# Kernel optimization log

Hardware: AMD Instinct MI355X
Metric: run time of the kernel (lower is better)

The kernel has to match this reference:

```python
import jax, jax.numpy as jnp
import numpy as np

B, T, I, H, L, O = 256, 256, 512, 1024, 2, 5


def setup_inputs() -> dict:
    key = jax.random.key(0)
    ks = jax.random.split(key, 8)
    x = jax.random.normal(ks[0], (B, T, I), dtype=jnp.float32)
    hidden = jnp.zeros((L, 2, B, H), dtype=jnp.float32)  # [layer, (h,c), B, H]
    # per-layer stacked gate weights: [4(gates f,i,g,o), H, in+H]
    W0 = jax.random.normal(ks[1], (4, H, I + H), dtype=jnp.float32) * 0.01
    b0 = jnp.zeros((4, H), dtype=jnp.float32)
    W1 = jax.random.normal(ks[2], (4, H, H + H), dtype=jnp.float32) * 0.01
    b1 = jnp.zeros((4, H), dtype=jnp.float32)
    W_out = jax.random.normal(ks[3], (O, H), dtype=jnp.float32) * 0.01
    b_out = jnp.zeros((O,), dtype=jnp.float32)
    return {"x": x, "hidden": hidden, "W0": W0, "b0": b0,
            "W1": W1, "b1": b1, "W_out": W_out, "b_out": b_out}


def _lstm_cell(W, b):
    # W: [4, H, in+H], gates in order (f, i, g, o) matching the torch module
    def cell(carry, x_t):
        h, c = carry
        combined = jnp.concatenate([h, x_t], axis=1)        # [B, H+in]
        gates = jnp.einsum('bk,ghk->gbh', combined, W) + b[:, None, :]
        f = jax.nn.sigmoid(gates[0])
        i = jax.nn.sigmoid(gates[1])
        g = jnp.tanh(gates[2])
        o = jax.nn.sigmoid(gates[3])
        c_new = f * c + i * g
        h_new = o * jnp.tanh(c_new)
        return (h_new, c_new), h_new
    return cell


def reference(x, hidden, W0, b0, W1, b1, W_out, b_out):
    xs = jnp.swapaxes(x, 0, 1)  # [T, B, I]
    finals = []
    for layer, (W, b) in enumerate([(W0, b0), (W1, b1)]):
        h0, c0 = hidden[layer, 0], hidden[layer, 1]
        (hT, cT), ys = jax.lax.scan(_lstm_cell(W, b), (h0, c0), xs)
        xs = ys                      # feed this layer's h sequence to next layer
        finals.append(jnp.stack([hT, cT]))
    last_hidden = xs[-1]             # [B, H], last timestep of top layer
    output = last_hidden @ W_out.T + b_out
    return output, jnp.stack(finals)  # ([B,O], [L,2,B,H])
```

## Files before the change

kernel.cpp:

```cpp
#include <hip/hip_runtime.h>
#include <hip/hip_bf16.h>
#include <cstdint>
#include <cstddef>

#define Bdim 256
#define Tdim 256
#define Idim 512
#define Hdim 1024
#define Odim 5
#define BH (Bdim * Hdim)

using short8 = __attribute__((ext_vector_type(8))) short;
using f32x4  = __attribute__((ext_vector_type(4))) float;
typedef unsigned long long u64;

__device__ __forceinline__ short bf16_of(float f) {
  unsigned u = __builtin_bit_cast(unsigned, f);
  u += 0x7fffu + ((u >> 16) & 1u);
  return (short)(u >> 16);
}

__device__ __forceinline__ float sigmf(float x) {
  return 1.0f / (1.0f + __expf(-x));
}

__global__ __launch_bounds__(256) void k_cvt_x(const float* __restrict__ src,
                                               short* __restrict__ dst) {
  int e = (blockIdx.x * 256 + threadIdx.x) * 8;
  int row = e >> 9;
  int i0  = e & 511;
  int b = row >> 8, t = row & 255;
  float4 u = *reinterpret_cast<const float4*>(src + e);
  float4 v = *reinterpret_cast<const float4*>(src + e + 4);
  short8 o = {bf16_of(u.x), bf16_of(u.y), bf16_of(u.z), bf16_of(u.w),
              bf16_of(v.x), bf16_of(v.y), bf16_of(v.z), bf16_of(v.w)};
  *reinterpret_cast<short8*>(dst + (((t << 8) + b) << 9) + i0) = o;
}

__global__ __launch_bounds__(256) void k_init(const float* __restrict__ hidden,
    short* __restrict__ h0s0, short* __restrict__ h1s0) {
  int i = blockIdx.x * 256 + threadIdx.x;
  if (i < BH) {
    h0s0[i] = bf16_of(hidden[i]);
    h1s0[i] = bf16_of(hidden[2 * BH + i]);
  }
}

__device__ __forceinline__ void ctr_arrive(unsigned* ctr, int c) {
  __builtin_amdgcn_sched_barrier(0);
  __syncthreads();
  if (threadIdx.x == 0)
    __hip_atomic_fetch_add(&ctr[c * 32], 1u, __ATOMIC_RELAXED,
                           __HIP_MEMORY_SCOPE_AGENT);
}

__device__ __forceinline__ void ctr_poll2(unsigned* ctr, unsigned tg0, unsigned tg1) {
  if (threadIdx.x < 64) {
    const int lane = threadIdx.x;
    const unsigned tgt = (lane < 8) ? tg0 : (lane < 16 ? tg1 : 0u);
    unsigned* p = ctr + (lane < 16 ? lane : 0) * 32;
    for (;;) {
      bool ok = true;
      if (tgt) {
        unsigned v = __hip_atomic_load(p, __ATOMIC_RELAXED, __HIP_MEMORY_SCOPE_AGENT);
        ok = (v >= tgt);
      }
      if (__all(ok)) break;
      __builtin_amdgcn_s_sleep(1);
    }
  }
}

#define LOADBLK(SUF, A0P, A1P, KB)                                             \
  { _Pragma("unroll")                                                          \
    for (int u = 0; u < 8; ++u) {                                              \
      const int k = (KB) + u * 32 + kl;                                        \
      Ar0##SUF[u] = *(const short8*)((A0P) + k);                               \
      Ar1##SUF[u] = *(const short8*)((A1P) + k);                               \
      Br0##SUF[u] = *(const short8*)(lb0 + k);                                 \
      Br1##SUF[u] = *(const short8*)(lb1 + k);                                 \
    } }

#define MFMABLK(SUF)                                                           \
  { _Pragma("unroll")                                                          \
    for (int u = 0; u < 8; ++u) {                                              \
      acc[0][0] = __builtin_amdgcn_mfma_f32_16x16x32_bf16(Ar0##SUF[u], Br0##SUF[u], acc[0][0], 0, 0, 0); \
      acc[1][0] = __builtin_amdgcn_mfma_f32_16x16x32_bf16(Ar1##SUF[u], Br0##SUF[u], acc[1][0], 0, 0, 0); \
      acc[0][1] = __builtin_amdgcn_mfma_f32_16x16x32_bf16(Ar0##SUF[u], Br1##SUF[u], acc[0][1], 0, 0, 0); \
      acc[1][1] = __builtin_amdgcn_mfma_f32_16x16x32_bf16(Ar1##SUF[u], Br1##SUF[u], acc[1][1], 0, 0, 0); \
    } }

#define GEMM_SEG4(P0, P1, KB)                                                  \
  LOADBLK(A, P0, P1, (KB))                                                     \
  LOADBLK(B, P0, P1, (KB) + 256)                                               \
  MFMABLK(A)                                                                   \
  LOADBLK(A, P0, P1, (KB) + 512)                                               \
  MFMABLK(B)                                                                   \
  LOADBLK(B, P0, P1, (KB) + 768)                                               \
  MFMABLK(A)                                                                   \
  MFMABLK(B)

#define GEMM_X(XF0, XF1)                                                       \
  for (int blk = 0; blk < 4; ++blk) {                                          \
    f32x4 U0[4][2], U1[4][2]; short8 Bx0[4], Bx1[4];                           \
    const int kb = Hdim + blk * 128 + kl;                                      \
    _Pragma("unroll")                                                          \
    for (int u = 0; u < 4; ++u) {                                              \
      const int k = kb + u * 32;                                               \
      U0[u][0] = *(const f32x4*)((XF0) + k);                                   \
      U0[u][1] = *(const f32x4*)((XF0) + k + 4);                               \
      U1[u][0] = *(const f32x4*)((XF1) + k);                                   \
      U1[u][1] = *(const f32x4*)((XF1) + k + 4);                               \
      Bx0[u] = *(const short8*)(lb0 + k);                                      \
      Bx1[u] = *(const short8*)(lb1 + k);                                      \
    }                                                                          \
    _Pragma("unroll")                                                          \
    for (int u = 0; u < 4; ++u) {                                              \
      short8 a0 = {bf16_of(U0[u][0][0]), bf16_of(U0[u][0][1]), bf16_of(U0[u][0][2]), bf16_of(U0[u][0][3]), \
                   bf16_of(U0[u][1][0]), bf16_of(U0[u][1][1]), bf16_of(U0[u][1][2]), bf16_of(U0[u][1][3])}; \
      short8 a1 = {bf16_of(U1[u][0][0]), bf16_of(U1[u][0][1]), bf16_of(U1[u][0][2]), bf16_of(U1[u][0][3]), \
                   bf16_of(U1[u][1][0]), bf16_of(U1[u][1][1]), bf16_of(U1[u][1][2]), bf16_of(U1[u][1][3])}; \
      acc[0][0] = __builtin_amdgcn_mfma_f32_16x16x32_bf16(a0, Bx0[u], acc[0][0], 0, 0, 0); \
      acc[1][0] = __builtin_amdgcn_mfma_f32_16x16x32_bf16(a1, Bx0[u], acc[1][0], 0, 0, 0); \
      acc[0][1] = __builtin_amdgcn_mfma_f32_16x16x32_bf16(a0, Bx1[u], acc[0][1], 0, 0, 0); \
      acc[1][1] = __builtin_amdgcn_mfma_f32_16x16x32_bf16(a1, Bx1[u], acc[1][1], 0, 0, 0); \
    }                                                                          \
  }

__global__ __launch_bounds__(512, 1) void k_persist(
    const float* __restrict__ W0, const float* __restrict__ b0v,
    const float* __restrict__ W1, const float* __restrict__ b1v,
    const float* __restrict__ hidden,
    const float* __restrict__ xf,
    const short* __restrict__ xbt,
    int useXb,
    short* __restrict__ h0seq,
    short* __restrict__ h1seq,
    float* __restrict__ finals,
    unsigned* __restrict__ ctr, int D) {
  extern __shared__ short lw[];
  const int tid  = threadIdx.x;
  const int wg   = blockIdx.x;
  const bool isL0 = (wg < 128);
  const int slot  = isL0 ? wg : wg - 128;
  const int hcol0 = slot * 8;
  const int K     = isL0 ? (Hdim + Idim) : (2 * Hdim);
  const int pitch = K + 8;
  const int layer = isL0 ? 0 : 1;
  const int myc   = layer * 8 + (wg & 7);
  const int lead  = (D > 4) ? (D - 2) : 2;
  const float* Wsrc = isL0 ? W0 : W1;
  const float* bsrc = isL0 ? b0v : b1v;

  for (int r = 0; r < 32; ++r) {
    const float* src = Wsrc + (size_t)((r >> 3) * Hdim + hcol0 + (r & 7)) * K;
    short* dst = lw + r * pitch;
    for (int k = tid; k < K; k += 512) dst[k] = bf16_of(src[k]);
  }

  const int lane = tid & 63;
  const int wv   = tid >> 6;
  const int col  = lane & 15;
  const int rg   = lane >> 4;
  const int kl   = rg * 8;
  const int row0 = wv * 32 + col;

  float biasv[2];
  #pragma unroll
  for (int n = 0; n < 2; ++n)
    biasv[n] = bsrc[(n * 2 + (col >= 8 ? 1 : 0)) * Hdim + hcol0 + (col & 7)];

  float creg[2][4], hfin[2][4];
  #pragma unroll
  for (int m = 0; m < 2; ++m)
    #pragma unroll
    for (int j = 0; j < 4; ++j) {
      int b = wv * 32 + m * 16 + rg * 4 + j;
      creg[m][j] = hidden[(layer * 2 + 1) * BH + b * Hdim + hcol0 + (col & 7)];
      hfin[m][j] = 0.f;
    }

  if (tid == 0)
    (void)__hip_atomic_load(ctr, __ATOMIC_ACQUIRE, __HIP_MEMORY_SCOPE_AGENT);
  __syncthreads();

  const short* lb0 = lw + col * pitch;
  const short* lb1 = lw + (16 + col) * pitch;

  int i_cur = 0;
  for (int r = 0; r < 256; ++r) {
    const int i_next = (i_cur + 1 == D) ? 0 : i_cur + 1;
    f32x4 acc[2][2] = {};
    short8 Ar0A[8], Ar1A[8], Br0A[8], Br1A[8];
    short8 Ar0B[8], Ar1B[8], Br0B[8], Br1B[8];
    short* hout;

    if (isL0) {
      if (useXb) {
        const short* xa = xbt + (size_t)r * (Bdim * Idim) + row0 * Idim - Hdim;
        const short* xc = xa + 16 * Idim;
        LOADBLK(A, xa, xc, 1024)
        LOADBLK(B, xa, xc, 1280)
        MFMABLK(A)
        MFMABLK(B)
      } else {
        const float* xf0 = xf + (size_t)(row0 * Tdim + r) * Idim - Hdim;
        const float* xf1 = xf + (size_t)((row0 + 16) * Tdim + r) * Idim - Hdim;
        GEMM_X(xf0, xf1)
      }
      __builtin_amdgcn_sched_barrier(0);
      unsigned tg1 = (r > lead) ? 16u * (unsigned)(r - lead) : 0u;
      if (r > 0 || tg1) ctr_poll2(ctr, 16u * (unsigned)r, tg1);
      if (tid == 0 && r > 0 && i_cur == 0)
        (void)__hip_atomic_load(ctr, __ATOMIC_ACQUIRE, __HIP_MEMORY_SCOPE_AGENT);
      __syncthreads();
      const short* ah = h0seq + (size_t)i_cur * BH + row0 * Hdim;
      GEMM_SEG4(ah, ah + 16 * Hdim, 0)
      hout = h0seq + (size_t)i_next * BH;
    } else {
      if (r > 0) ctr_poll2(ctr, 0u, 16u * (unsigned)r);
      if (tid == 0 && r > 0 && i_cur == 0)
        (void)__hip_atomic_load(ctr, __ATOMIC_ACQUIRE, __HIP_MEMORY_SCOPE_AGENT);
      __syncthreads();
      const short* ah = h1seq + (size_t)i_cur * BH + row0 * Hdim;
      GEMM_SEG4(ah, ah + 16 * Hdim, 0)
      __builtin_amdgcn_sched_barrier(0);
      ctr_poll2(ctr, 16u * (unsigned)(r + 1), 0u);
      __syncthreads();
      const short* ax = h0seq + (size_t)i_next * BH + row0 * Hdim - Hdim;
      GEMM_SEG4(ax, ax + 16 * Hdim, 1024)
      hout = h1seq + (size_t)i_next * BH;
    }

    #pragma unroll
    for (int m = 0; m < 2; ++m) {
      #pragma unroll
      for (int j = 0; j < 4; ++j) {
        float fi  = acc[m][0][j] + biasv[0];
        float go  = acc[m][1][j] + biasv[1];
        float iv_ = __shfl_xor(fi, 8, 64);
        float ov_ = __shfl_xor(go, 8, 64);
        float fv = sigmf(fi), iv = sigmf(iv_);
        float gv = tanhf(go), ov = sigmf(ov_);
        float cn = fv * creg[m][j] + iv * gv;
        creg[m][j] = cn;
        float hn = ov * tanhf(cn);
        hfin[m][j] = hn;
        unsigned hv = (unsigned)(unsigned short)bf16_of(hn);
        unsigned p1 = hv | ((unsigned)__shfl_xor((int)hv, 1, 64) << 16);
        u64 p2 = (u64)p1 | ((u64)(unsigned)__shfl_xor((int)p1, 2, 64) << 32);
        if ((col & 3) == 0 && col < 8) {
          int b = wv * 32 + m * 16 + rg * 4 + j;
          __hip_atomic_store((u64*)(hout + b * Hdim + hcol0 + col), p2,
                             __ATOMIC_RELAXED, __HIP_MEMORY_SCOPE_AGENT);
        }
      }
    }
    ctr_arrive(ctr, myc);
    i_cur = i_next;
  }

  if (col < 8) {
    #pragma unroll
    for (int m = 0; m < 2; ++m)
      #pragma unroll
      for (int j = 0; j < 4; ++j) {
        int b = wv * 32 + m * 16 + rg * 4 + j;
        finals[(layer * 2 + 0) * BH + b * Hdim + hcol0 + col] = hfin[m][j];
        finals[(layer * 2 + 1) * BH + b * Hdim + hcol0 + col] = creg[m][j];
      }
  }
}

__global__ __launch_bounds__(256) void k_outproj(const float* __restrict__ h1f,
    const float* __restrict__ Wout, const float* __restrict__ bout,
    float* __restrict__ out) {
  int b = blockIdx.x;
  int tid = threadIdx.x;
  float hv[4];
  #pragma unroll
  for (int j = 0; j < 4; ++j) hv[j] = h1f[b * Hdim + tid + j * 256];
  __shared__ float red[Odim][4];
  #pragma unroll
  for (int o = 0; o < Odim; ++o) {
    float p = 0.f;
    #pragma unroll
    for (int j = 0; j < 4; ++j) p += hv[j] * Wout[o * Hdim + tid + j * 256];
    #pragma unroll
    for (int s = 32; s > 0; s >>= 1) p += __shfl_down(p, s, 64);
    if ((tid & 63) == 0) red[o][tid >> 6] = p;
  }
  __syncthreads();
  if (tid < Odim)
    out[b * Odim + tid] = red[tid][0] + red[tid][1] + red[tid][2] + red[tid][3] + bout[tid];
}

extern "C" void kernel_launch(void* const* d_in, const int* in_sizes, int n_in,
                              void* d_out, int out_size, void* d_ws, size_t ws_size,
                              hipStream_t stream) {
  const float* x      = (const float*)d_in[0];
  const float* hidden = (const float*)d_in[1];
  const float* W0     = (const float*)d_in[2];
  const float* b0     = (const float*)d_in[3];
  const float* W1     = (const float*)d_in[4];
  const float* b1     = (const float*)d_in[5];
  const float* Wout   = (const float*)d_in[6];
  const float* bout   = (const float*)d_in[7];
  float* out = (float*)d_out;
  float* finals = out + Bdim * Odim;

  char* ws = (char*)d_ws;
  size_t off = 0;
  auto alloc = [&](size_t bytes) {
    void* p = ws + off;
    off += (bytes + 255) & ~(size_t)255;
    return p;
  };
  unsigned* ctr = (unsigned*)alloc(16 * 32 * sizeof(unsigned));
  const size_t seqSlot = (size_t)BH * 2;
  const size_t xbBytes = (size_t)Tdim * Bdim * Idim * 2;
  int useXb = 0;
  short* xbt = nullptr;
  if (ws_size > off + xbBytes + 8 * 2 * seqSlot + (1 << 20)) {
    useXb = 1;
    xbt = (short*)alloc(xbBytes);
  }
  size_t avail = (ws_size > off + 512) ? (ws_size - off - 512) : 0;
  int D = (int)(avail / (2 * seqSlot));
  if (D > 257) D = 257;
  if (D < 4) D = 4;
  short* h0seq = (short*)alloc((size_t)D * seqSlot);
  short* h1seq = (short*)alloc((size_t)D * seqSlot);

  if (useXb)
    k_cvt_x<<<(Tdim * Bdim * Idim) / (256 * 8), 256, 0, stream>>>(x, xbt);
  k_init<<<BH / 256, 256, 0, stream>>>(hidden, h0seq, h1seq);
  hipMemsetAsync(ctr, 0, 16 * 32 * sizeof(unsigned), stream);

  const int ldsBytes = 32 * (2 * Hdim + 8) * 2;
  hipFuncSetAttribute((const void*)k_persist,
                      hipFuncAttributeMaxDynamicSharedMemorySize, ldsBytes);
  void* args[] = {(void*)&W0, (void*)&b0, (void*)&W1, (void*)&b1,
                  (void*)&hidden, (void*)&x, (void*)&xbt, (void*)&useXb,
                  (void*)&h0seq, (void*)&h1seq,
                  (void*)&finals, (void*)&ctr, (void*)&D};
  hipLaunchCooperativeKernel((const void*)k_persist, dim3(256), dim3(512),
                             args, ldsBytes, stream);

  k_outproj<<<Bdim, 256, 0, stream>>>(finals + 2 * BH, Wout, bout, out);
}
```

Before: 8.399 ms.

## Stream activations into LDS via async global_load_lds and read weights from global

Weights are pre-converted to bf16 in a separate kernel and read directly from global (L2) per step instead of being held in LDS. Activation tiles (h and x sequences) are staged into a double-buffered per-wave LDS region using global_load_lds with explicit vmcnt waits, pipelining loads with MFMA. Layer-1 synchronization is merged into a single poll before the step, and the ring depth D is capped at 64. This aims to overlap global traffic with compute, at the cost of re-reading weights from L2 every timestep and losing the earlier overlap of the x-projection with the wait.

New measurement: 15.41 ms. 1.83x slower.

```diff
diff --git a/kernel.cpp b/kernel.cpp
--- a/kernel.cpp
+++ b/kernel.cpp
@@ -9,6 +9,7 @@
 #define Hdim 1024
 #define Odim 5
 #define BH (Bdim * Hdim)
+#define BI (Bdim * Idim)
 
 using short8 = __attribute__((ext_vector_type(8))) short;
 using f32x4  = __attribute__((ext_vector_type(4))) float;
@@ -22,6 +23,19 @@
 
 __device__ __forceinline__ float sigmf(float x) {
   return 1.0f / (1.0f + __expf(-x));
+}
+
+__global__ __launch_bounds__(256) void k_cvt_bf16(const float* __restrict__ src,
+                                                  short* __restrict__ dst, int n) {
+  int i0 = (blockIdx.x * 256 + threadIdx.x) * 8;
+  int stride = gridDim.x * 256 * 8;
+  for (int i = i0; i < n; i += stride) {
+    float4 u = *reinterpret_cast<const float4*>(src + i);
+    float4 v = *reinterpret_cast<const float4*>(src + i + 4);
+    short8 o = {bf16_of(u.x), bf16_of(u.y), bf16_of(u.z), bf16_of(u.w),
+                bf16_of(v.x), bf16_of(v.y), bf16_of(v.z), bf16_of(v.w)};
+    *reinterpret_cast<short8*>(dst + i) = o;
+  }
 }
 
 __global__ __launch_bounds__(256) void k_cvt_x(const float* __restrict__ src,
@@ -71,65 +85,23 @@
   }
 }
 
-#define LOADBLK(SUF, A0P, A1P, KB)                                             \
-  { _Pragma("unroll")                                                          \
-    for (int u = 0; u < 8; ++u) {                                              \
-      const int k = (KB) + u * 32 + kl;                                        \
-      Ar0##SUF[u] = *(const short8*)((A0P) + k);                               \
-      Ar1##SUF[u] = *(const short8*)((A1P) + k);                               \
-      Br0##SUF[u] = *(const short8*)(lb0 + k);                                 \
-      Br1##SUF[u] = *(const short8*)(lb1 + k);                                 \
-    } }
-
-#define MFMABLK(SUF)                                                           \
-  { _Pragma("unroll")                                                          \
-    for (int u = 0; u < 8; ++u) {                                              \
-      acc[0][0] = __builtin_amdgcn_mfma_f32_16x16x32_bf16(Ar0##SUF[u], Br0##SUF[u], acc[0][0], 0, 0, 0); \
-      acc[1][0] = __builtin_amdgcn_mfma_f32_16x16x32_bf16(Ar1##SUF[u], Br0##SUF[u], acc[1][0], 0, 0, 0); \
-      acc[0][1] = __builtin_amdgcn_mfma_f32_16x16x32_bf16(Ar0##SUF[u], Br1##SUF[u], acc[0][1], 0, 0, 0); \
-      acc[1][1] = __builtin_amdgcn_mfma_f32_16x16x32_bf16(Ar1##SUF[u], Br1##SUF[u], acc[1][1], 0, 0, 0); \
-    } }
-
-#define GEMM_SEG4(P0, P1, KB)                                                  \
-  LOADBLK(A, P0, P1, (KB))                                                     \
-  LOADBLK(B, P0, P1, (KB) + 256)                                               \
-  MFMABLK(A)                                                                   \
-  LOADBLK(A, P0, P1, (KB) + 512)                                               \
-  MFMABLK(B)                                                                   \
-  LOADBLK(B, P0, P1, (KB) + 768)                                               \
-  MFMABLK(A)                                                                   \
-  MFMABLK(B)
-
-#define GEMM_X(XF0, XF1)                                                       \
-  for (int blk = 0; blk < 4; ++blk) {                                          \
-    f32x4 U0[4][2], U1[4][2]; short8 Bx0[4], Bx1[4];                           \
-    const int kb = Hdim + blk * 128 + kl;                                      \
-    _Pragma("unroll")                                                          \
-    for (int u = 0; u < 4; ++u) {                                              \
-      const int k = kb + u * 32;                                               \
-      U0[u][0] = *(const f32x4*)((XF0) + k);                                   \
-      U0[u][1] = *(const f32x4*)((XF0) + k + 4);                               \
-      U1[u][0] = *(const f32x4*)((XF1) + k);                                   \
-      U1[u][1] = *(const f32x4*)((XF1) + k + 4);                               \
-      Bx0[u] = *(const short8*)(lb0 + k);                                      \
-      Bx1[u] = *(const short8*)(lb1 + k);                                      \
-    }                                                                          \
-    _Pragma("unroll")                                                          \
-    for (int u = 0; u < 4; ++u) {                                              \
-      short8 a0 = {bf16_of(U0[u][0][0]), bf16_of(U0[u][0][1]), bf16_of(U0[u][0][2]), bf16_of(U0[u][0][3]), \
-                   bf16_of(U0[u][1][0]), bf16_of(U0[u][1][1]), bf16_of(U0[u][1][2]), bf16_of(U0[u][1][3])}; \
-      short8 a1 = {bf16_of(U1[u][0][0]), bf16_of(U1[u][0][1]), bf16_of(U1[u][0][2]), bf16_of(U1[u][0][3]), \
-                   bf16_of(U1[u][1][0]), bf16_of(U1[u][1][1]), bf16_of(U1[u][1][2]), bf16_of(U1[u][1][3])}; \
-      acc[0][0] = __builtin_amdgcn_mfma_f32_16x16x32_bf16(a0, Bx0[u], acc[0][0], 0, 0, 0); \
-      acc[1][0] = __builtin_amdgcn_mfma_f32_16x16x32_bf16(a1, Bx0[u], acc[1][0], 0, 0, 0); \
-      acc[0][1] = __builtin_amdgcn_mfma_f32_16x16x32_bf16(a0, Bx1[u], acc[0][1], 0, 0, 0); \
-      acc[1][1] = __builtin_amdgcn_mfma_f32_16x16x32_bf16(a1, Bx1[u], acc[1][1], 0, 0, 0); \
-    }                                                                          \
-  }
+__device__ __forceinline__ void stage_super(short* sb, const short* g, int rs, int l) {
+  #pragma unroll
+  for (int j = 0; j < 8; ++j) {
+    const int row = l & 31;
+    const int kb  = j * 2 + (l >> 5);
+    const short* src = g + (size_t)row * rs + kb * 8;
+    __builtin_amdgcn_global_load_lds(
+        (const __attribute__((address_space(1))) unsigned int*)(const void*)src,
+        (__attribute__((address_space(3))) unsigned int*)(void*)(sb + j * 512),
+        16, 0, 0);
+  }
+}
 
 __global__ __launch_bounds__(512, 1) void k_persist(
-    const float* __restrict__ W0, const float* __restrict__ b0v,
-    const float* __restrict__ W1, const float* __restrict__ b1v,
+    const short* __restrict__ W0b,
+    const short* __restrict__ W1b,
+    const float* __restrict__ b0v, const float* __restrict__ b1v,
     const float* __restrict__ hidden,
     const float* __restrict__ xf,
     const short* __restrict__ xbt,
@@ -145,25 +117,21 @@
   const int slot  = isL0 ? wg : wg - 128;
   const int hcol0 = slot * 8;
   const int K     = isL0 ? (Hdim + Idim) : (2 * Hdim);
-  const int pitch = K + 8;
   const int layer = isL0 ? 0 : 1;
   const int myc   = layer * 8 + (wg & 7);
-  const int lead  = (D > 4) ? (D - 2) : 2;
-  const float* Wsrc = isL0 ? W0 : W1;
+  const int lead  = D - 2;
+  const short* Wb = isL0 ? W0b : W1b;
   const float* bsrc = isL0 ? b0v : b1v;
-
-  for (int r = 0; r < 32; ++r) {
-    const float* src = Wsrc + (size_t)((r >> 3) * Hdim + hcol0 + (r & 7)) * K;
-    short* dst = lw + r * pitch;
-    for (int k = tid; k < K; k += 512) dst[k] = bf16_of(src[k]);
-  }
 
   const int lane = tid & 63;
   const int wv   = tid >> 6;
   const int col  = lane & 15;
   const int rg   = lane >> 4;
   const int kl   = rg * 8;
-  const int row0 = wv * 32 + col;
+  const int wv32 = wv * 32;
+
+  const short* wrow0 = Wb + (size_t)((col >> 3) * Hdim + hcol0 + (col & 7)) * K;
+  const short* wrow1 = Wb + (size_t)((2 + (col >> 3)) * Hdim + hcol0 + (col & 7)) * K;
 
   float biasv[2];
   #pragma unroll
@@ -175,7 +143,7 @@
   for (int m = 0; m < 2; ++m)
     #pragma unroll
     for (int j = 0; j < 4; ++j) {
-      int b = wv * 32 + m * 16 + rg * 4 + j;
+      int b = wv32 + m * 16 + rg * 4 + j;
       creg[m][j] = hidden[(layer * 2 + 1) * BH + b * Hdim + hcol0 + (col & 7)];
       hfin[m][j] = 0.f;
     }
@@ -184,54 +152,99 @@
     (void)__hip_atomic_load(ctr, __ATOMIC_ACQUIRE, __HIP_MEMORY_SCOPE_AGENT);
   __syncthreads();
 
-  const short* lb0 = lw + col * pitch;
-  const short* lb1 = lw + (16 + col) * pitch;
+  short* ab0 = lw + wv * 8192;
+  short* ab1 = ab0 + 4096;
 
   int i_cur = 0;
   for (int r = 0; r < 256; ++r) {
     const int i_next = (i_cur + 1 == D) ? 0 : i_cur + 1;
+
+    if (isL0) {
+      unsigned tg1 = (r > lead) ? 16u * (unsigned)(r - lead) : 0u;
+      if (r > 0 || tg1) ctr_poll2(ctr, (r > 0) ? 16u * (unsigned)r : 0u, tg1);
+    } else {
+      ctr_poll2(ctr, 16u * (unsigned)(r + 1), (r > 0) ? 16u * (unsigned)r : 0u);
+    }
+    if (tid == 0 && r > 0 && (i_cur == 0 || i_next == 0))
+      (void)__hip_atomic_load(ctr, __ATOMIC_ACQUIRE, __HIP_MEMORY_SCOPE_AGENT);
+    __syncthreads();
+
+    const int NS = isL0 ? (useXb ? 12 : 8) : 16;
+    const short* sA = (isL0 ? h0seq + (size_t)i_cur * BH
+                            : h1seq + (size_t)i_cur * BH) + (size_t)wv32 * Hdim;
+    const short* sX = isL0 ? (useXb ? xbt + (size_t)r * BI + (size_t)wv32 * Idim
+                                    : (const short*)nullptr)
+                           : h0seq + (size_t)i_next * BH + (size_t)wv32 * Hdim;
+    const int rsX = isL0 ? Idim : Hdim;
+
     f32x4 acc[2][2] = {};
-    short8 Ar0A[8], Ar1A[8], Br0A[8], Br1A[8];
-    short8 Ar0B[8], Ar1B[8], Br0B[8], Br1B[8];
-    short* hout;
-
-    if (isL0) {
-      if (useXb) {
-        const short* xa = xbt + (size_t)r * (Bdim * Idim) + row0 * Idim - Hdim;
-        const short* xc = xa + 16 * Idim;
-        LOADBLK(A, xa, xc, 1024)
-        LOADBLK(B, xa, xc, 1280)
-        MFMABLK(A)
-        MFMABLK(B)
-      } else {
-        const float* xf0 = xf + (size_t)(row0 * Tdim + r) * Idim - Hdim;
-        const float* xf1 = xf + (size_t)((row0 + 16) * Tdim + r) * Idim - Hdim;
-        GEMM_X(xf0, xf1)
-      }
+    short8 Bc0[4], Bc1[4], Bn0[4], Bn1[4];
+
+    stage_super(ab0, sA, Hdim, lane);
+    stage_super(ab1, sA + 128, Hdim, lane);
+    #pragma unroll
+    for (int t = 0; t < 4; ++t) {
+      Bc0[t] = *(const short8*)(wrow0 + t * 32 + kl);
+      Bc1[t] = *(const short8*)(wrow1 + t * 32 + kl);
+    }
+
+    for (int s = 0; s < NS; ++s) {
+      if (s == NS - 1) { asm volatile("s_waitcnt vmcnt(8)" ::: "memory"); }
+      else             { asm volatile("s_waitcnt vmcnt(16)" ::: "memory"); }
       __builtin_amdgcn_sched_barrier(0);
-      unsigned tg1 = (r > lead) ? 16u * (unsigned)(r - lead) : 0u;
-      if (r > 0 || tg1) ctr_poll2(ctr, 16u * (unsigned)r, tg1);
-      if (tid == 0 && r > 0 && i_cur == 0)
-        (void)__hip_atomic_load(ctr, __ATOMIC_ACQUIRE, __HIP_MEMORY_SCOPE_AGENT);
-      __syncthreads();
-      const short* ah = h0seq + (size_t)i_cur * BH + row0 * Hdim;
-      GEMM_SEG4(ah, ah + 16 * Hdim, 0)
-      hout = h0seq + (size_t)i_next * BH;
-    } else {
-      if (r > 0) ctr_poll2(ctr, 0u, 16u * (unsigned)r);
-      if (tid == 0 && r > 0 && i_cur == 0)
-        (void)__hip_atomic_load(ctr, __ATOMIC_ACQUIRE, __HIP_MEMORY_SCOPE_AGENT);
-      __syncthreads();
-      const short* ah = h1seq + (size_t)i_cur * BH + row0 * Hdim;
-      GEMM_SEG4(ah, ah + 16 * Hdim, 0)
+
+      if (s + 1 < NS) {
+        const int kg = (s + 1) * 128 + kl;
+        #pragma unroll
+        for (int t = 0; t < 4; ++t) {
+          Bn0[t] = *(const short8*)(wrow0 + kg + t * 32);
+          Bn1[t] = *(const short8*)(wrow1 + kg + t * 32);
+        }
+      }
+
+      const short* sb = (s & 1) ? ab1 : ab0;
+      #pragma unroll
+      for (int t = 0; t < 4; ++t) {
+        const short8 a0 = *(const short8*)(sb + (t * 4 + rg) * 256 + col * 8);
+        const short8 a1 = *(const short8*)(sb + (t * 4 + rg) * 256 + (16 + col) * 8);
+        acc[0][0] = __builtin_amdgcn_mfma_f32_16x16x32_bf16(a0, Bc0[t], acc[0][0], 0, 0, 0);
+        acc[1][0] = __builtin_amdgcn_mfma_f32_16x16x32_bf16(a1, Bc0[t], acc[1][0], 0, 0, 0);
+        acc[0][1] = __builtin_amdgcn_mfma_f32_16x16x32_bf16(a0, Bc1[t], acc[0][1], 0, 0, 0);
+        acc[1][1] = __builtin_amdgcn_mfma_f32_16x16x32_bf16(a1, Bc1[t], acc[1][1], 0, 0, 0);
+      }
+
+      asm volatile("s_waitcnt lgkmcnt(0)" ::: "memory");
       __builtin_amdgcn_sched_barrier(0);
-      ctr_poll2(ctr, 16u * (unsigned)(r + 1), 0u);
-      __syncthreads();
-      const short* ax = h0seq + (size_t)i_next * BH + row0 * Hdim - Hdim;
-      GEMM_SEG4(ax, ax + 16 * Hdim, 1024)
-      hout = h1seq + (size_t)i_next * BH;
-    }
-
+      if (s + 2 < NS) {
+        const int sn = s + 2;
+        const short* g = (sn < 8) ? sA + sn * 128 : sX + (sn - 8) * 128;
+        stage_super((s & 1) ? ab1 : ab0, g, (sn < 8) ? Hdim : rsX, lane);
+      }
+      #pragma unroll
+      for (int t = 0; t < 4; ++t) { Bc0[t] = Bn0[t]; Bc1[t] = Bn1[t]; }
+    }
+
+    if (isL0 && !useXb) {
+      const float* xf0 = xf + ((size_t)(wv32 + col) * Tdim + r) * Idim - Hdim;
+      const float* xf1 = xf + ((size_t)(wv32 + 16 + col) * Tdim + r) * Idim - Hdim;
+      for (int k0 = Hdim; k0 < K; k0 += 32) {
+        int k = k0 + kl;
+        short8 b0 = *(const short8*)(wrow0 + k);
+        short8 b1 = *(const short8*)(wrow1 + k);
+        f32x4 u0 = *(const f32x4*)(xf0 + k), u1 = *(const f32x4*)(xf0 + k + 4);
+        f32x4 v0 = *(const f32x4*)(xf1 + k), v1 = *(const f32x4*)(xf1 + k + 4);
+        short8 a0 = {bf16_of(u0[0]), bf16_of(u0[1]), bf16_of(u0[2]), bf16_of(u0[3]),
+                     bf16_of(u1[0]), bf16_of(u1[1]), bf16_of(u1[2]), bf16_of(u1[3])};
+        short8 a1 = {bf16_of(v0[0]), bf16_of(v0[1]), bf16_of(v0[2]), bf16_of(v0[3]),
+                     bf16_of(v1[0]), bf16_of(v1[1]), bf16_of(v1[2]), bf16_of(v1[3])};
+        acc[0][0] = __builtin_amdgcn_mfma_f32_16x16x32_bf16(a0, b0, acc[0][0], 0, 0, 0);
+        acc[1][0] = __builtin_amdgcn_mfma_f32_16x16x32_bf16(a1, b0, acc[1][0], 0, 0, 0);
+        acc[0][1] = __builtin_amdgcn_mfma_f32_16x16x32_bf16(a0, b1, acc[0][1], 0, 0, 0);
+        acc[1][1] = __builtin_amdgcn_mfma_f32_16x16x32_bf16(a1, b1, acc[1][1], 0, 0, 0);
+      }
+    }
+
+    short* hout = isL0 ? h0seq + (size_t)i_next * BH : h1seq + (size_t)i_next * BH;
     #pragma unroll
     for (int m = 0; m < 2; ++m) {
       #pragma unroll
@@ -250,7 +263,7 @@
         unsigned p1 = hv | ((unsigned)__shfl_xor((int)hv, 1, 64) << 16);
         u64 p2 = (u64)p1 | ((u64)(unsigned)__shfl_xor((int)p1, 2, 64) << 32);
         if ((col & 3) == 0 && col < 8) {
-          int b = wv * 32 + m * 16 + rg * 4 + j;
+          int b = wv32 + m * 16 + rg * 4 + j;
           __hip_atomic_store((u64*)(hout + b * Hdim + hcol0 + col), p2,
                              __ATOMIC_RELAXED, __HIP_MEMORY_SCOPE_AGENT);
         }
@@ -265,7 +278,7 @@
     for (int m = 0; m < 2; ++m)
       #pragma unroll
       for (int j = 0; j < 4; ++j) {
-        int b = wv * 32 + m * 16 + rg * 4 + j;
+        int b = wv32 + m * 16 + rg * 4 + j;
         finals[(layer * 2 + 0) * BH + b * Hdim + hcol0 + col] = hfin[m][j];
         finals[(layer * 2 + 1) * BH + b * Hdim + hcol0 + col] = creg[m][j];
       }
@@ -317,6 +330,8 @@
     return p;
   };
   unsigned* ctr = (unsigned*)alloc(16 * 32 * sizeof(unsigned));
+  short* W0b = (short*)alloc((size_t)4096 * 1536 * 2);
+  short* W1b = (short*)alloc((size_t)4096 * 2048 * 2);
   const size_t seqSlot = (size_t)BH * 2;
   const size_t xbBytes = (size_t)Tdim * Bdim * Idim * 2;
   int useXb = 0;
@@ -327,20 +342,22 @@
   }
   size_t avail = (ws_size > off + 512) ? (ws_size - off - 512) : 0;
   int D = (int)(avail / (2 * seqSlot));
-  if (D > 257) D = 257;
+  if (D > 64) D = 64;
   if (D < 4) D = 4;
   short* h0seq = (short*)alloc((size_t)D * seqSlot);
   short* h1seq = (short*)alloc((size_t)D * seqSlot);
 
+  k_cvt_bf16<<<2048, 256, 0, stream>>>(W0, W0b, 4096 * 1536);
+  k_cvt_bf16<<<2048, 256, 0, stream>>>(W1, W1b, 4096 * 2048);
   if (useXb)
     k_cvt_x<<<(Tdim * Bdim * Idim) / (256 * 8), 256, 0, stream>>>(x, xbt);
   k_init<<<BH / 256, 256, 0, stream>>>(hidden, h0seq, h1seq);
   hipMemsetAsync(ctr, 0, 16 * 32 * sizeof(unsigned), stream);
 
-  const int ldsBytes = 32 * (2 * Hdim + 8) * 2;
+  const int ldsBytes = 8 * 2 * 4096 * 2;
   hipFuncSetAttribute((const void*)k_persist,
                       hipFuncAttributeMaxDynamicSharedMemorySize, ldsBytes);
-  void* args[] = {(void*)&W0, (void*)&b0, (void*)&W1, (void*)&b1,
+  void* args[] = {(void*)&W0b, (void*)&W1b, (void*)&b0, (void*)&b1,
                   (void*)&hidden, (void*)&x, (void*)&xbt, (void*)&useXb,
                   (void*)&h0seq, (void*)&h1seq,
                   (void*)&finals, (void*)&ctr, (void*)&D};
```
